# Kernel optimization log

Hardware: AMD Instinct MI355X
Metric: run time of the kernel (lower is better)

Reference implementation:

```python
import jax, jax.numpy as jnp
import numpy as np

EPS = 1e-5
NUM_HEADS = 8
SCALE = 0.125


def _lin_bn_relu(x, w, b, g, beta, mu, var):
    # Linear (y = x @ w.T + b), BatchNorm1d over channel dim (eval-mode affine), ReLU
    y = jnp.einsum('bnc,dc->bnd', x, w) + b
    y = (y - mu) * (g / jnp.sqrt(var + EPS)) + beta
    return jax.nn.relu(y)


def setup_inputs() -> dict:
    key = jax.random.key(0)
    B, N, C = 8, 1024, 512
    keys = jax.random.split(key, 16)
    d = {'x': jax.random.normal(keys[0], (B, N, C), dtype=jnp.float32)}
    for i, p in enumerate(['q', 'k', 'v', 'p']):
        kw, kb, kmu = keys[1 + 3 * i], keys[2 + 3 * i], keys[3 + 3 * i]
        d[f'{p}_w'] = jax.random.normal(kw, (C, C), dtype=jnp.float32) * 0.02
        d[f'{p}_b'] = jnp.zeros((C,), dtype=jnp.float32)
        d[f'{p}_g'] = jnp.ones((C,), dtype=jnp.float32)
        d[f'{p}_beta'] = jnp.zeros((C,), dtype=jnp.float32)
        d[f'{p}_mu'] = jax.random.normal(kmu, (C,), dtype=jnp.float32) * 0.02
        d[f'{p}_var'] = jax.random.uniform(kb, (C,), dtype=jnp.float32, minval=0.5, maxval=1.5)
    return d


def reference(x,
              q_w, q_b, q_g, q_beta, q_mu, q_var,
              k_w, k_b, k_g, k_beta, k_mu, k_var,
              v_w, v_b, v_g, v_beta, v_mu, v_var,
              p_w, p_b, p_g, p_beta, p_mu, p_var):
    B, N, C = x.shape
    H = NUM_HEADS
    dh = C // H

    def heads(t):  # [B,N,C] -> [B,H,N,dh]
        return t.reshape(B, N, H, dh).transpose(0, 2, 1, 3)

    q = heads(_lin_bn_relu(x, q_w, q_b, q_g, q_beta, q_mu, q_var))
    k = heads(_lin_bn_relu(x, k_w, k_b, k_g, k_beta, k_mu, k_var))
    v = heads(_lin_bn_relu(x, v_w, v_b, v_g, v_beta, v_mu, v_var))

    attn = jnp.einsum('bhnd,bhmd->bhnm', q, k) * SCALE  # no softmax
    out = jnp.einsum('bhnm,bhmd->bhnd', attn, v)
    out = out.transpose(0, 2, 1, 3).reshape(B, N, C)
    out = jax.nn.relu(out)  # attn_lif
    return _lin_bn_relu(out, p_w, p_b, p_g, p_beta, p_mu, p_var)
```

## Files before the change

kernel.cpp:

```cpp
#include <hip/hip_runtime.h>


#define CDIM  512
#define NSEQ  1024
#define MROWS 8192

typedef __attribute__((ext_vector_type(8))) __bf16  bf16x8;
typedef __attribute__((ext_vector_type(4))) float   f32x4;
typedef __attribute__((ext_vector_type(8))) ushort  u16x8;

__device__ __forceinline__ float b2f(ushort u) {
    union { uint i; float f; } v; v.i = ((uint)u) << 16; return v.f;
}
__device__ __forceinline__ ushort f2b(float f) {
    union { float f; uint i; } v; v.f = f;
    uint u = v.i;
    u = u + 0x7fffu + ((u >> 16) & 1u);
    return (ushort)(u >> 16);
}
__device__ __forceinline__ float ldv(const void* p, long i, int f32) {
    return f32 ? ((const float*)p)[i] : b2f(((const ushort*)p)[i]);
}

__device__ __forceinline__ void gload16(const void* g, void* l) {
    __builtin_amdgcn_global_load_lds(
        (const __attribute__((address_space(1))) void*)g,
        (__attribute__((address_space(3))) void*)l,
        16, 0, 0);
}

struct BnArgs {
    const void* b[4]; const void* g[4]; const void* be[4];
    const void* mu[4]; const void* va[4];
};
struct WPtrs { const void* w[4]; };

__global__ __launch_bounds__(256) void prep_all(
    const void* __restrict__ x, WPtrs wp, BnArgs bn,
    ushort* __restrict__ Xb, ushort* __restrict__ Wb,
    float* __restrict__ s_all, float* __restrict__ t_all,
    float* __restrict__ S, int* __restrict__ flag)
{
    const int blk = blockIdx.x, t = threadIdx.x;
    if (blk >= 2568) {
        ((float4*)S)[(blk - 2568) * 256 + t] = make_float4(0.f, 0.f, 0.f, 0.f);
        return;
    }

    __shared__ int cnt;
    if (t == 0) cnt = 0;
    __syncthreads();
    {
        const ushort* xu = (const ushort*)x;
        int c = 0;
        for (int i = t; i < 2048; i += 256) {
            uint e = ((uint)xu[i] >> 7) & 0xffu;
            if (e >= 0xC8u) ++c;
        }
        if (c) atomicAdd(&cnt, c);
    }
    __syncthreads();
    const int f32 = cnt > 32;
    if (blk == 0 && t == 0) *flag = f32;

    if (blk < 2048) {
        long i = ((long)blk * 256 + t) * 8;
        if (f32) {
            const float* s = (const float*)x + i;
            u16x8 o;
            #pragma unroll
            for (int j = 0; j < 8; ++j) o[j] = f2b(s[j]);
            *(u16x8*)(Xb + i) = o;
        } else {
            *(u16x8*)(Xb + i) = *(const u16x8*)((const ushort*)x + i);
        }
    } else if (blk < 2560) {
        int bb = blk - 2048;
        int p = bb >> 7;
        long i = ((long)(bb & 127) * 256 + t) * 8;
        const void* src = wp.w[p];
        ushort* d = Wb + (long)p * 262144 + i;
        if (f32) {
            const float* s = (const float*)src + i;
            u16x8 o;
            #pragma unroll
            for (int j = 0; j < 8; ++j) o[j] = f2b(s[j]);
            *(u16x8*)d = o;
        } else {
            *(u16x8*)d = *(const u16x8*)((const ushort*)src + i);
        }
    } else {
        int idx = (blk - 2560) * 256 + t;
        int br = idx >> 9, c = idx & 511;
        float g  = ldv(bn.g[br],  c, f32);
        float be = ldv(bn.be[br], c, f32);
        float mu = ldv(bn.mu[br], c, f32);
        float va = ldv(bn.va[br], c, f32);
        float bb = ldv(bn.b[br],  c, f32);
        float s = g / sqrtf(va + 1e-5f);
        s_all[idx] = s;
        t_all[idx] = (bb - mu) * s + be;
    }
}

__device__ __forceinline__ void gemm128(
    const ushort* __restrict__ A, const ushort* __restrict__ Bw, void* __restrict__ O,
    const float* __restrict__ s_all, const float* __restrict__ t_all,
    int st_off, int of32)
{
    __shared__ ushort As[8192];
    __shared__ ushort Bs[8192];
    const int t = threadIdx.x;
    const int wave = t >> 6, lane = t & 63;
    const int wr = wave >> 1, wc = wave & 1;
    const long row0 = (long)blockIdx.x * 128;
    const int  col0 = blockIdx.y * 128;

    const ushort* gA = A  + (row0 + (t >> 3)) * CDIM + (t & 7) * 8;
    const ushort* gB = Bw + (long)(col0 + (t >> 3)) * CDIM + (t & 7) * 8;
    ushort* lA = As + wave * 512;
    ushort* lB = Bs + wave * 512;

    f32x4 acc[4][4] = {};

    for (int k0 = 0; k0 < CDIM; k0 += 64) {
        #pragma unroll
        for (int r = 0; r < 4; ++r) {
            gload16(gA + (long)r * 32 * CDIM + k0, lA + r * 2048);
            gload16(gB + (long)r * 32 * CDIM + k0, lB + r * 2048);
        }
        __syncthreads();

        #pragma unroll
        for (int ks = 0; ks < 2; ++ks) {
            bf16x8 av[4], bv[4];
            #pragma unroll
            for (int m = 0; m < 4; ++m)
                av[m] = *(const bf16x8*)&As[(wr * 64 + m * 16 + (lane & 15)) * 64 + ks * 32 + (lane >> 4) * 8];
            #pragma unroll
            for (int n = 0; n < 4; ++n)
                bv[n] = *(const bf16x8*)&Bs[(wc * 64 + n * 16 + (lane & 15)) * 64 + ks * 32 + (lane >> 4) * 8];
            #pragma unroll
            for (int m = 0; m < 4; ++m)
                #pragma unroll
                for (int n = 0; n < 4; ++n)
                    acc[m][n] = __builtin_amdgcn_mfma_f32_16x16x32_bf16(av[m], bv[n], acc[m][n], 0, 0, 0);
        }
        __syncthreads();
    }

    const int lr4 = (lane >> 4) * 4, lc = lane & 15;
    #pragma unroll
    for (int n = 0; n < 4; ++n) {
        const int col = col0 + wc * 64 + n * 16 + lc;
        const float s = s_all[st_off + col], tt = t_all[st_off + col];
        #pragma unroll
        for (int m = 0; m < 4; ++m) {
            const long rb = row0 + wr * 64 + m * 16 + lr4;
            #pragma unroll
            for (int i = 0; i < 4; ++i) {
                float v = acc[m][n][i] * s + tt;
                v = v > 0.f ? v : 0.f;
                if (of32) ((float*)O)[(rb + i) * CDIM + col] = v;
                else      ((ushort*)O)[(rb + i) * CDIM + col] = f2b(v);
            }
        }
    }
}

__global__ __launch_bounds__(256) void gemm_qkv(
    const ushort* __restrict__ Xb, const ushort* __restrict__ Wb,
    ushort* __restrict__ QKV,
    const float* __restrict__ s_all, const float* __restrict__ t_all)
{
    int z = blockIdx.z;
    gemm128(Xb, Wb + (long)z * 262144, QKV + (long)z * 4194304,
            s_all, t_all, z * 512, 0);
}

__global__ __launch_bounds__(256) void gemm_p(
    const ushort* __restrict__ Aq, const ushort* __restrict__ Wp,
    void* __restrict__ O,
    const float* __restrict__ s_all, const float* __restrict__ t_all,
    const int* __restrict__ flag)
{
    gemm128(Aq, Wp, O, s_all, t_all, 1536, *flag);
}

__global__ __launch_bounds__(256) void ktv_kernel(
    const ushort* __restrict__ K, const ushort* __restrict__ V,
    float* __restrict__ S)
{
    int bh = blockIdx.x, b = bh >> 3, h = bh & 7;
    int ns = blockIdx.y;
    __shared__ float Ks[32][64];
    __shared__ float Vs[32][64];
    int t = threadIdx.x;
    int lr = t >> 3, lc = (t & 7) * 8;
    int r0 = (t >> 4) * 4, c0 = (t & 15) * 4;
    const ushort* Kb = K + ((long)b * NSEQ + ns * 128) * CDIM + h * 64;
    const ushort* Vb = V + ((long)b * NSEQ + ns * 128) * CDIM + h * 64;

    float acc[4][4] = {};
    for (int it = 0; it < 4; ++it) {
        __syncthreads();
        long n = (long)(it * 32 + lr) * CDIM;
        u16x8 kv = *(const u16x8*)&Kb[n + lc];
        u16x8 vv = *(const u16x8*)&Vb[n + lc];
        #pragma unroll
        for (int j = 0; j < 8; ++j) {
            Ks[lr][lc + j] = b2f(kv[j]);
            Vs[lr][lc + j] = b2f(vv[j]);
        }
        __syncthreads();
        #pragma unroll
        for (int nn = 0; nn < 32; ++nn) {
            f32x4 kf = *(const f32x4*)&Ks[nn][r0];
            f32x4 vf = *(const f32x4*)&Vs[nn][c0];
            #pragma unroll
            for (int i = 0; i < 4; ++i)
                #pragma unroll
                for (int j = 0; j < 4; ++j)
                    acc[i][j] += kf[i] * vf[j];
        }
    }
    float* out = S + ((long)bh * 64 + r0) * 64 + c0;
    #pragma unroll
    for (int i = 0; i < 4; ++i)
        #pragma unroll
        for (int j = 0; j < 4; ++j)
            atomicAdd(&out[i * 64 + j], acc[i][j]);
}

__global__ __launch_bounds__(256) void attn_kernel(
    ushort* __restrict__ Q, const float* __restrict__ S)
{
    int bh = blockIdx.x, b = bh >> 3, h = bh & 7;
    int m0 = blockIdx.y * 64;
    __shared__ float Ss[64][64];
    __shared__ float Qs[64][68];
    int t = threadIdx.x, ty = t >> 4, tx = t & 15;

    for (int e = t; e < 4096; e += 256)
        Ss[e >> 6][e & 63] = S[(long)bh * 4096 + e];
    ushort* Qb = Q + ((long)(b * NSEQ + m0)) * CDIM + h * 64;
    for (int e = t; e < 4096; e += 256) {
        int r = e >> 6, c = e & 63;
        Qs[c][r] = b2f(Qb[(long)r * CDIM + c]);
    }
    __syncthreads();

    float acc[4][4] = {};
    for (int d1 = 0; d1 < 64; ++d1) {
        f32x4 qv = *(const f32x4*)&Qs[d1][ty * 4];
        f32x4 sv = *(const f32x4*)&Ss[d1][tx * 4];
        #pragma unroll
        for (int i = 0; i < 4; ++i)
            #pragma unroll
            for (int j = 0; j < 4; ++j)
                acc[i][j] += qv[i] * sv[j];
    }
    #pragma unroll
    for (int i = 0; i < 4; ++i) {
        ushort4 o;
        o.x = f2b(fmaxf(0.125f * acc[i][0], 0.f));
        o.y = f2b(fmaxf(0.125f * acc[i][1], 0.f));
        o.z = f2b(fmaxf(0.125f * acc[i][2], 0.f));
        o.w = f2b(fmaxf(0.125f * acc[i][3], 0.f));
        *(ushort4*)&Qb[(long)(ty * 4 + i) * CDIM + tx * 4] = o;
    }
}

extern "C" void kernel_launch(void* const* d_in, const int* in_sizes, int n_in,
                              void* d_out, int out_size, void* d_ws, size_t ws_size,
                              hipStream_t stream)
{
    const void* x = d_in[0];
    WPtrs wp; BnArgs bn;
    for (int p = 0; p < 4; ++p) {
        wp.w[p]   = d_in[1 + 6 * p + 0];
        bn.b[p]   = d_in[1 + 6 * p + 1];
        bn.g[p]   = d_in[1 + 6 * p + 2];
        bn.be[p]  = d_in[1 + 6 * p + 3];
        bn.mu[p]  = d_in[1 + 6 * p + 4];
        bn.va[p]  = d_in[1 + 6 * p + 5];
    }

    char* ws = (char*)d_ws;
    float*  s_all = (float*)ws;
    float*  t_all = (float*)(ws + 8192);
    int*    flag  = (int*)(ws + 16384);
    ushort* Wb    = (ushort*)(ws + 16640);
    ushort* QKV   = (ushort*)(ws + 16640 + 2097152);
    float*  S     = (float*)(ws + 16640 + 2097152 + 3L * 8388608);
    ushort* Xb    = (ushort*)d_out;

    prep_all<<<2824, 256, 0, stream>>>(x, wp, bn, Xb, Wb, s_all, t_all, S, flag);

    gemm_qkv<<<dim3(64, 4, 3), 256, 0, stream>>>(Xb, Wb, QKV, s_all, t_all);

    ktv_kernel<<<dim3(64, 8), 256, 0, stream>>>(QKV + 4194304, QKV + 2L * 4194304, S);

    attn_kernel<<<dim3(64, 16), 256, 0, stream>>>(QKV, S);

    gemm_p<<<dim3(64, 4), 256, 0, stream>>>(QKV, Wb + 3L * 262144, d_out,
                                            s_all, t_all, flag);
}
```

Measured before the change: 200.5 us.

## Double-buffer GEMM LDS tiles and replace atomic KtV reduction with partial sums

```diff
diff --git a/kernel.cpp b/kernel.cpp
--- a/kernel.cpp
+++ b/kernel.cpp
@@ -39,13 +39,9 @@
     const void* __restrict__ x, WPtrs wp, BnArgs bn,
     ushort* __restrict__ Xb, ushort* __restrict__ Wb,
     float* __restrict__ s_all, float* __restrict__ t_all,
-    float* __restrict__ S, int* __restrict__ flag)
+    int* __restrict__ flag)
 {
     const int blk = blockIdx.x, t = threadIdx.x;
-    if (blk >= 2568) {
-        ((float4*)S)[(blk - 2568) * 256 + t] = make_float4(0.f, 0.f, 0.f, 0.f);
-        return;
-    }
 
     __shared__ int cnt;
     if (t == 0) cnt = 0;
@@ -108,8 +104,8 @@
     const float* __restrict__ s_all, const float* __restrict__ t_all,
     int st_off, int of32)
 {
-    __shared__ ushort As[8192];
-    __shared__ ushort Bs[8192];
+    __shared__ ushort As[2][8192];
+    __shared__ ushort Bs[2][8192];
     const int t = threadIdx.x;
     const int wave = t >> 6, lane = t & 63;
     const int wr = wave >> 1, wc = wave & 1;
@@ -118,28 +114,34 @@
 
     const ushort* gA = A  + (row0 + (t >> 3)) * CDIM + (t & 7) * 8;
     const ushort* gB = Bw + (long)(col0 + (t >> 3)) * CDIM + (t & 7) * 8;
-    ushort* lA = As + wave * 512;
-    ushort* lB = Bs + wave * 512;
+
+    auto STAGE = [&](int b, int k0) {
+        #pragma unroll
+        for (int r = 0; r < 4; ++r) {
+            gload16(gA + (long)r * 32 * CDIM + k0, &As[b][r * 2048 + wave * 512]);
+            gload16(gB + (long)r * 32 * CDIM + k0, &Bs[b][r * 2048 + wave * 512]);
+        }
+    };
 
     f32x4 acc[4][4] = {};
 
-    for (int k0 = 0; k0 < CDIM; k0 += 64) {
-        #pragma unroll
-        for (int r = 0; r < 4; ++r) {
-            gload16(gA + (long)r * 32 * CDIM + k0, lA + r * 2048);
-            gload16(gB + (long)r * 32 * CDIM + k0, lB + r * 2048);
-        }
-        __syncthreads();
+    STAGE(0, 0);
+    __syncthreads();
+
+    #pragma unroll
+    for (int kt = 0; kt < 8; ++kt) {
+        const int cur = kt & 1;
+        if (kt < 7) STAGE(cur ^ 1, (kt + 1) * 64);
 
         #pragma unroll
         for (int ks = 0; ks < 2; ++ks) {
             bf16x8 av[4], bv[4];
             #pragma unroll
             for (int m = 0; m < 4; ++m)
-                av[m] = *(const bf16x8*)&As[(wr * 64 + m * 16 + (lane & 15)) * 64 + ks * 32 + (lane >> 4) * 8];
+                av[m] = *(const bf16x8*)&As[cur][(wr * 64 + m * 16 + (lane & 15)) * 64 + ks * 32 + (lane >> 4) * 8];
             #pragma unroll
             for (int n = 0; n < 4; ++n)
-                bv[n] = *(const bf16x8*)&Bs[(wc * 64 + n * 16 + (lane & 15)) * 64 + ks * 32 + (lane >> 4) * 8];
+                bv[n] = *(const bf16x8*)&Bs[cur][(wc * 64 + n * 16 + (lane & 15)) * 64 + ks * 32 + (lane >> 4) * 8];
             #pragma unroll
             for (int m = 0; m < 4; ++m)
                 #pragma unroll
@@ -189,7 +191,7 @@
 
 __global__ __launch_bounds__(256) void ktv_kernel(
     const ushort* __restrict__ K, const ushort* __restrict__ V,
-    float* __restrict__ S)
+    float* __restrict__ Spart)
 {
     int bh = blockIdx.x, b = bh >> 3, h = bh & 7;
     int ns = blockIdx.y;
@@ -224,16 +226,16 @@
                     acc[i][j] += kf[i] * vf[j];
         }
     }
-    float* out = S + ((long)bh * 64 + r0) * 64 + c0;
+    float* out = Spart + ((long)bh * 8 + ns) * 4096 + r0 * 64 + c0;
     #pragma unroll
     for (int i = 0; i < 4; ++i)
         #pragma unroll
         for (int j = 0; j < 4; ++j)
-            atomicAdd(&out[i * 64 + j], acc[i][j]);
+            out[i * 64 + j] = acc[i][j];
 }
 
 __global__ __launch_bounds__(256) void attn_kernel(
-    ushort* __restrict__ Q, const float* __restrict__ S)
+    ushort* __restrict__ Q, const float* __restrict__ Spart)
 {
     int bh = blockIdx.x, b = bh >> 3, h = bh & 7;
     int m0 = blockIdx.y * 64;
@@ -241,8 +243,13 @@
     __shared__ float Qs[64][68];
     int t = threadIdx.x, ty = t >> 4, tx = t & 15;
 
-    for (int e = t; e < 4096; e += 256)
-        Ss[e >> 6][e & 63] = S[(long)bh * 4096 + e];
+    for (int e = t; e < 4096; e += 256) {
+        const float* sp = Spart + (long)bh * 32768 + e;
+        float v = 0.f;
+        #pragma unroll
+        for (int ns = 0; ns < 8; ++ns) v += sp[ns * 4096];
+        Ss[e >> 6][e & 63] = v;
+    }
     ushort* Qb = Q + ((long)(b * NSEQ + m0)) * CDIM + h * 64;
     for (int e = t; e < 4096; e += 256) {
         int r = e >> 6, c = e & 63;
@@ -292,16 +299,16 @@
     int*    flag  = (int*)(ws + 16384);
     ushort* Wb    = (ushort*)(ws + 16640);
     ushort* QKV   = (ushort*)(ws + 16640 + 2097152);
-    float*  S     = (float*)(ws + 16640 + 2097152 + 3L * 8388608);
+    float*  Spart = (float*)(ws + 16640 + 2097152 + 3L * 8388608);
     ushort* Xb    = (ushort*)d_out;
 
-    prep_all<<<2824, 256, 0, stream>>>(x, wp, bn, Xb, Wb, s_all, t_all, S, flag);
+    prep_all<<<2568, 256, 0, stream>>>(x, wp, bn, Xb, Wb, s_all, t_all, flag);
 
     gemm_qkv<<<dim3(64, 4, 3), 256, 0, stream>>>(Xb, Wb, QKV, s_all, t_all);
 
-    ktv_kernel<<<dim3(64, 8), 256, 0, stream>>>(QKV + 4194304, QKV + 2L * 4194304, S);
-
-    attn_kernel<<<dim3(64, 16), 256, 0, stream>>>(QKV, S);
+    ktv_kernel<<<dim3(64, 8), 256, 0, stream>>>(QKV + 4194304, QKV + 2L * 4194304, Spart);
+
+    attn_kernel<<<dim3(64, 16), 256, 0, stream>>>(QKV, Spart);
 
     gemm_p<<<dim3(64, 4), 256, 0, stream>>>(QKV, Wb + 3L * 262144, d_out,
                                             s_all, t_all, flag);
```

Result: faster. 187.3 us (-6.6%).
